# Performance work log

Measured on AMD Instinct MI355X. Metric: run time of the kernel, lower is better.

Reference implementation:

```python
import jax, jax.numpy as jnp
import numpy as np

D = 512          # hidden_dim
H_HEADS = 8
DH = D // H_HEADS  # 64
L = 6            # n_layers
P = 8            # patch size
KT = 3           # temporal kernel
Z_DIM = 32
FILM_SCALE = 0.5
ROPE_BASE = 10000.0
EPS = 1e-5


def layer_norm(x, g, b):
    mu = x.mean(-1, keepdims=True)
    var = ((x - mu) ** 2).mean(-1, keepdims=True)
    return (x - mu) * jax.lax.rsqrt(var + EPS) * g + b


def rotate_half(x):
    x1, x2 = jnp.split(x, 2, axis=-1)
    return jnp.concatenate([-x2, x1], axis=-1)


def rope_time(T, dtype):
    half = DH // 2
    inv_freq = ROPE_BASE ** (-(jnp.arange(half, dtype=dtype) / half))  # (half,)
    angles = jnp.arange(T, dtype=dtype)[:, None] * inv_freq[None, :]   # (T, half)
    sin = jnp.concatenate([jnp.sin(angles), jnp.sin(angles)], -1)      # (T, DH)
    cos = jnp.concatenate([jnp.cos(angles), jnp.cos(angles)], -1)
    return sin, cos


def setup_inputs() -> dict:
    key = jax.random.key(0)
    ks = iter(jax.random.split(key, 64))
    n = lambda shape, s=0.02: jax.random.normal(next(ks), shape, jnp.float32) * s
    inp = {
        "x": jax.random.normal(next(ks), (16, 32, 3, 64, 64), jnp.float32),
        "z": jax.random.normal(next(ks), (16, 32, Z_DIM), jnp.float32),
        # tokenizer: CausalConv3d (kt,ph,pw)=(3,8,8), stride (1,8,8)
        "conv_w": n((D, 3, KT, P, P)),
        "conv_b": jnp.zeros((D,), jnp.float32),
        "tok_g": jnp.ones((D,), jnp.float32),
        "tok_b": jnp.zeros((D,), jnp.float32),
        # FiLM from z -> (gamma, beta)
        "film_w": n((Z_DIM, 2 * D)),
        "film_b": jnp.zeros((2 * D,), jnp.float32),
        # transformer blocks (stacked over L)
        "ln1_g": jnp.ones((L, D), jnp.float32), "ln1_b": jnp.zeros((L, D), jnp.float32),
        "kqv_w": n((L, D, 3 * D)), "kqv_b": jnp.zeros((L, 3 * D), jnp.float32),
        "proj_w": n((L, D, D)), "proj_b": jnp.zeros((L, D), jnp.float32),
        "ln2_g": jnp.ones((L, D), jnp.float32), "ln2_b": jnp.zeros((L, D), jnp.float32),
        "mlp_w1": n((L, D, 4 * D)), "mlp_b1": jnp.zeros((L, 4 * D), jnp.float32),
        "mlp_w2": n((L, 4 * D, D)), "mlp_b2": jnp.zeros((L, D), jnp.float32),
        "rs_attn": jnp.full((L,), 0.5, jnp.float32),
        "rs_mlp": jnp.full((L,), 0.5, jnp.float32),
        # scoring head
        "head_g": jnp.ones((D,), jnp.float32), "head_b": jnp.zeros((D,), jnp.float32),
        "head_w": n((D, 1)), "head_bias": jnp.zeros((1,), jnp.float32),
    }
    return inp


def _forward(x, z, conv_w, conv_b, tok_g, tok_b, film_w, film_b,
             ln1_g, ln1_b, kqv_w, kqv_b, proj_w, proj_b, ln2_g, ln2_b,
             mlp_w1, mlp_b1, mlp_w2, mlp_b2, rs_attn, rs_mlp,
             head_g, head_b, head_w, head_bias):
    B, T, C, Himg, Wimg = x.shape
    # ---- SpatialTemporalTokenizer: causal Conv3d (pad time on past only) ----
    xc = jnp.transpose(x, (0, 2, 1, 3, 4))  # [B,C,T,H,W]
    y = jax.lax.conv_general_dilated(
        xc, conv_w, window_strides=(1, P, P),
        padding=[(KT - 1, 0), (0, 0), (0, 0)],
        dimension_numbers=("NCDHW", "OIDHW", "NCDHW"))
    y = y + conv_b[None, :, None, None, None]          # [B,D,T,Hn,Wn]
    Hn, Wn = y.shape[3], y.shape[4]
    tok = jnp.transpose(y, (0, 2, 3, 4, 1)).reshape(B, T, Hn * Wn, D)
    tok = layer_norm(tok, tok_g, tok_b)                 # [B,T,N,D]
    # ---- FiLM conditioning from z ----
    gb = z @ film_w + film_b                            # [B,T,2D]
    gamma, beta = jnp.split(gb, 2, axis=-1)
    tok = (1.0 + FILM_SCALE * gamma)[:, :, None, :] * tok + (FILM_SCALE * beta)[:, :, None, :]
    # ---- spatial pooling -> temporal sequence ----
    h = tok.mean(axis=2)                                # [B,T,D]
    # ---- transformer stack (causal, time RoPE, pre-LN, gated residuals) ----
    sin_t, cos_t = rope_time(T, h.dtype)                # (T, DH)
    causal = jnp.tril(jnp.ones((T, T), bool))
    neg_inf = jnp.finfo(h.dtype).min
    for i in range(L):
        xi = layer_norm(h, ln1_g[i], ln1_b[i])
        kqv = xi @ kqv_w[i] + kqv_b[i]                  # [B,T,3D]
        k, q, v = jnp.split(kqv, 3, axis=-1)            # torch chunk order: k,q,v
        sh = lambda t: t.reshape(B, T, H_HEADS, DH).transpose(0, 2, 1, 3)  # [B,h,T,d]
        q, k, v = sh(q), sh(k), sh(v)
        q = q * cos_t + rotate_half(q) * sin_t
        k = k * cos_t + rotate_half(k) * sin_t
        att = jnp.einsum("bhqd,bhkd->bhqk", q, k) / np.sqrt(DH)
        att = jnp.where(causal[None, None], att, neg_inf)
        att = jax.nn.softmax(att, axis=-1)
        yv = jnp.einsum("bhqk,bhkd->bhqd", att, v)
        yv = yv.transpose(0, 2, 1, 3).reshape(B, T, D)
        attn_out = yv @ proj_w[i] + proj_b[i]
        h = h + rs_attn[i] * attn_out
        x2 = layer_norm(h, ln2_g[i], ln2_b[i])
        m = jax.nn.gelu(x2 @ mlp_w1[i] + mlp_b1[i], approximate=False) @ mlp_w2[i] + mlp_b2[i]
        h = h + rs_mlp[i] * m
    # ---- per-timestep score head ----
    h = layer_norm(h, head_g, head_b)
    score = (h @ head_w + head_bias)[..., 0]            # [B,T]
    return score


def reference(x, z, conv_w, conv_b, tok_g, tok_b, film_w, film_b,
              ln1_g, ln1_b, kqv_w, kqv_b, proj_w, proj_b, ln2_g, ln2_b,
              mlp_w1, mlp_b1, mlp_w2, mlp_b2, rs_attn, rs_mlp,
              head_g, head_b, head_w, head_bias):
    return _forward(x, z, conv_w, conv_b, tok_g, tok_b, film_w, film_b,
                    ln1_g, ln1_b, kqv_w, kqv_b, proj_w, proj_b, ln2_g, ln2_b,
                    mlp_w1, mlp_b1, mlp_w2, mlp_b2, rs_attn, rs_mlp,
                    head_g, head_b, head_w, head_bias)
```

## Files before the change

kernel.cpp:

```cpp
#include <hip/hip_runtime.h>
#include <math.h>

#define EPS 1e-5f

typedef __attribute__((ext_vector_type(8))) short short8;
typedef __attribute__((ext_vector_type(4))) float f32x4;

__device__ __forceinline__ short f2bf(float f) {
    unsigned u = __float_as_uint(f);
    u += 0x7fffu + ((u >> 16) & 1u);
    return (short)(u >> 16);
}
__device__ __forceinline__ float bf2f(short s) {
    return __uint_as_float(((unsigned)(unsigned short)s) << 16);
}
__device__ __forceinline__ void async16(const void* g, void* l) {
    __builtin_amdgcn_global_load_lds(
        (const __attribute__((address_space(1))) unsigned*)g,
        (__attribute__((address_space(3))) unsigned*)l, 16, 0, 0);
}

__device__ __forceinline__ float block_reduce_sum_256(float v, float* red) {
    #pragma unroll
    for (int o = 32; o > 0; o >>= 1) v += __shfl_down(v, o, 64);
    __syncthreads();
    if ((threadIdx.x & 63) == 0) red[threadIdx.x >> 6] = v;
    __syncthreads();
    return red[0] + red[1] + red[2] + red[3];
}

__global__ __launch_bounds__(256) void prep_all(
    const float* __restrict__ z, const float* __restrict__ fw,
    const float* __restrict__ fb, float* __restrict__ gb,
    const float* __restrict__ conv_w, short* __restrict__ wbf,
    const float* __restrict__ x, short* __restrict__ xbf,
    float* __restrict__ ropeS, float* __restrict__ ropeC,
    const float* __restrict__ kqv_w, short* __restrict__ kqvT,
    const float* __restrict__ proj_w, short* __restrict__ projT,
    const float* __restrict__ mlp_w1, short* __restrict__ mlp1T,
    const float* __restrict__ mlp_w2, short* __restrict__ mlp2T) {
    int bi = blockIdx.x, tid = threadIdx.x;
    if (bi < 512) {
        __shared__ float zs[32];
        if (tid < 32) zs[tid] = z[bi * 32 + tid];
        __syncthreads();
        for (int j = tid; j < 1024; j += 256) {
            float acc = fb[j];
            #pragma unroll
            for (int k = 0; k < 32; k++) acc = fmaf(zs[k], fw[k * 1024 + j], acc);
            gb[bi * 1024 + j] = acc;
        }
        return;
    }
    if (bi < 1664) {
        int i = (bi - 512) * 256 + tid;
        wbf[i] = f2bf(conv_w[i]);
        return;
    }
    if (bi < 4736) {
        int i = (bi - 1664) * 256 + tid;
        float4 a = *(const float4*)(x + (size_t)i * 8);
        float4 b = *(const float4*)(x + (size_t)i * 8 + 4);
        short8 o = {f2bf(a.x), f2bf(a.y), f2bf(a.z), f2bf(a.w),
                    f2bf(b.x), f2bf(b.y), f2bf(b.z), f2bf(b.w)};
        *(short8*)(xbf + (size_t)i * 8) = o;
        return;
    }
    if (bi < 4740) {
        int idx = (bi - 4736) * 256 + tid;
        if (idx < 1024) {
            int t = idx >> 5, j = idx & 31;
            float ang = (float)t * expf(-(float)j * (logf(10000.f) / 32.f));
            ropeS[idx] = sinf(ang);
            ropeC[idx] = cosf(ang);
        }
        return;
    }
    __shared__ float tile[32][33];
    int rel0 = bi - 4740;
    const float* src; short* dst; int NT, K, N, rel;
    if (rel0 < 4608)       { src = kqv_w;  dst = kqvT;  NT = 48; K = 512;  N = 1536; rel = rel0; }
    else if (rel0 < 6144)  { src = proj_w; dst = projT; NT = 16; K = 512;  N = 512;  rel = rel0 - 4608; }
    else if (rel0 < 12288) { src = mlp_w1; dst = mlp1T; NT = 64; K = 512;  N = 2048; rel = rel0 - 6144; }
    else                   { src = mlp_w2; dst = mlp2T; NT = 16; K = 2048; N = 512;  rel = rel0 - 12288; }
    int per = NT * (K / 32);
    int layer = rel / per, r2 = rel - layer * per;
    int nt = r2 % NT, kt = r2 / NT;
    src += (size_t)layer * K * N;
    dst += (size_t)layer * N * K;
    int n0 = nt * 32, k0 = kt * 32;
    int lx = tid & 31, ly = tid >> 5;
    #pragma unroll
    for (int i = 0; i < 32; i += 8)
        tile[ly + i][lx] = src[(size_t)(k0 + ly + i) * N + n0 + lx];
    __syncthreads();
    if (tid < 128) {
        int row = tid >> 2, c = tid & 3;
        short8 o;
        #pragma unroll
        for (int j = 0; j < 8; j++) o[j] = f2bf(tile[c * 8 + j][row]);
        *(short8*)(dst + (size_t)(n0 + row) * K + k0 + c * 8) = o;
    }
}

__global__ __launch_bounds__(256, 2) void conv_fused(
    const short* __restrict__ xbf, const short* __restrict__ wbf,
    const float* __restrict__ cb, const float* __restrict__ tg,
    const float* __restrict__ tb, const float* __restrict__ gb,
    float* __restrict__ h) {
    __shared__ short As[64 * 32];
    __shared__ short Bs[512 * 32];
    __shared__ float redsum[4][64], redss[4][64];
    __shared__ float mu_s[64], inv_s[64];
    int bt = blockIdx.x, b = bt >> 5, t = bt & 31;
    int tid = threadIdx.x;
    int wave = tid >> 6, lane = tid & 63, quad = lane >> 4, l16 = lane & 15;

    int rowA = tid >> 2;
    int cA = (tid & 3) ^ ((rowA >> 1) & 3);
    int hn = rowA >> 3, wn2 = rowA & 7;
    long long baseA = (((long long)(b * 32 + t - 2) * 3) << 12)
                      + (long long)(hn * 8) * 64 + wn2 * 8;

    f32x4 acc[4][8];
    #pragma unroll
    for (int mt = 0; mt < 4; mt++)
        #pragma unroll
        for (int nt = 0; nt < 8; nt++) acc[mt][nt] = (f32x4){0.f, 0.f, 0.f, 0.f};

    for (int k0 = 0; k0 < 576; k0 += 32) {
        #pragma unroll
        for (int e = 0; e < 8; e++) {
            int s = e * 256 + tid;
            int n = s >> 2;
            int c = (s & 3) ^ ((n >> 1) & 3);
            async16(wbf + (size_t)n * 576 + k0 + c * 8, Bs + s * 8);
        }
        {
            int ks = (k0 >> 3) + cA;
            int ch = (ks >= 24) + (ks >= 48);
            int r = ks - ch * 24;
            int kt = r >> 3, ph = r & 7;
            short8 v8 = (short8){0, 0, 0, 0, 0, 0, 0, 0};
            if (t + kt >= 2)
                v8 = *(const short8*)(xbf + baseA
                        + ((long long)(kt * 3 + ch) << 12) + ph * 64);
            *(short8*)(As + tid * 8) = v8;
        }
        __syncthreads();
        short8 af[4], bf[8];
        #pragma unroll
        for (int mt = 0; mt < 4; mt++) {
            int row = mt * 16 + l16;
            int pc = quad ^ ((row >> 1) & 3);
            af[mt] = *(const short8*)(As + row * 32 + pc * 8);
        }
        #pragma unroll
        for (int nt = 0; nt < 8; nt++) {
            int row = wave * 128 + nt * 16 + l16;
            int pc = quad ^ ((row >> 1) & 3);
            bf[nt] = *(const short8*)(Bs + row * 32 + pc * 8);
        }
        #pragma unroll
        for (int mt = 0; mt < 4; mt++)
            #pragma unroll
            for (int nt = 0; nt < 8; nt++)
                acc[mt][nt] = __builtin_amdgcn_mfma_f32_16x16x32_bf16(
                    af[mt], bf[nt], acc[mt][nt], 0, 0, 0);
        __syncthreads();
    }

    float cbn[8], tgn[8], tbn[8], Gn[8], Ben[8];
    #pragma unroll
    for (int nt = 0; nt < 8; nt++) {
        int n = wave * 128 + nt * 16 + l16;
        cbn[nt] = cb[n]; tgn[nt] = tg[n]; tbn[nt] = tb[n];
        Gn[nt]  = 1.f + 0.5f * gb[bt * 1024 + n];
        Ben[nt] = 0.5f * gb[bt * 1024 + 512 + n];
    }
    #pragma unroll
    for (int mt = 0; mt < 4; mt++)
        #pragma unroll
        for (int reg = 0; reg < 4; reg++) {
            float s = 0.f, ss = 0.f;
            #pragma unroll
            for (int nt = 0; nt < 8; nt++) {
                float v = acc[mt][nt][reg] + cbn[nt];
                s += v; ss += v * v;
            }
            #pragma unroll
            for (int o = 1; o < 16; o <<= 1) {
                s  += __shfl_xor(s, o, 64);
                ss += __shfl_xor(ss, o, 64);
            }
            if (l16 == 0) {
                int m = mt * 16 + quad * 4 + reg;
                redsum[wave][m] = s; redss[wave][m] = ss;
            }
        }
    __syncthreads();
    if (tid < 64) {
        float S  = redsum[0][tid] + redsum[1][tid] + redsum[2][tid] + redsum[3][tid];
        float SS = redss[0][tid] + redss[1][tid] + redss[2][tid] + redss[3][tid];
        float mu = S * (1.f / 512.f);
        float var = SS * (1.f / 512.f) - mu * mu;
        mu_s[tid] = mu; inv_s[tid] = rsqrtf(var + EPS);
    }
    __syncthreads();
    float hacc[8] = {0.f, 0.f, 0.f, 0.f, 0.f, 0.f, 0.f, 0.f};
    #pragma unroll
    for (int mt = 0; mt < 4; mt++)
        #pragma unroll
        for (int reg = 0; reg < 4; reg++) {
            int m = mt * 16 + quad * 4 + reg;
            float mu = mu_s[m], inv = inv_s[m];
            #pragma unroll
            for (int nt = 0; nt < 8; nt++) {
                float v = acc[mt][nt][reg] + cbn[nt];
                hacc[nt] += (v - mu) * inv;
            }
        }
    #pragma unroll
    for (int nt = 0; nt < 8; nt++) {
        hacc[nt] += __shfl_xor(hacc[nt], 16, 64);
        hacc[nt] += __shfl_xor(hacc[nt], 32, 64);
    }
    if (quad == 0)
        #pragma unroll
        for (int nt = 0; nt < 8; nt++) {
            int n = wave * 128 + nt * 16 + l16;
            h[bt * 512 + n] = Gn[nt] * (tgn[nt] * (hacc[nt] * (1.f / 64.f)) + tbn[nt])
                              + Ben[nt];
        }
}

__global__ __launch_bounds__(256) void attn_fused(
    const float* __restrict__ hsrc, const float* __restrict__ lng,
    const float* __restrict__ lnb, const short* __restrict__ Bw,
    const float* __restrict__ bias, const float* __restrict__ ropeS,
    const float* __restrict__ ropeC, short* __restrict__ yv) {
    __shared__ char smem[57344] __attribute__((aligned(16)));
    __shared__ float mu_s[32], inv_s[32];
    short* As = (short*)smem;
    short* BsB[2] = {(short*)(smem + 32768), (short*)(smem + 45056)};
    float (*qsf)[64] = (float(*)[64])(smem);
    float (*ksf)[64] = (float(*)[64])(smem + 8192);
    short* vT  = (short*)(smem + 16384);
    short* qrb = (short*)(smem + 20480);
    short* krb = (short*)(smem + 24576);
    float (*att)[33] = (float(*)[33])(smem + 28672);
    short* pA  = (short*)(smem + 36864);
    int blk = blockIdx.x, b = blk >> 3, hh = blk & 7;
    int tid = threadIdx.x;
    int m0 = b * 32;
    {
        int row = tid >> 3, l8 = tid & 7;
        const float* hp = hsrc + (size_t)(m0 + row) * 512 + l8 * 64;
        float s = 0.f, ss = 0.f;
        #pragma unroll
        for (int i = 0; i < 16; i++) {
            float4 v = *(const float4*)(hp + i * 4);
            s += v.x + v.y + v.z + v.w;
            ss += v.x * v.x + v.y * v.y + v.z * v.z + v.w * v.w;
        }
        s += __shfl_xor(s, 1, 64); ss += __shfl_xor(ss, 1, 64);
        s += __shfl_xor(s, 2, 64); ss += __shfl_xor(ss, 2, 64);
        s += __shfl_xor(s, 4, 64); ss += __shfl_xor(ss, 4, 64);
        if (l8 == 0) {
            float mu = s * (1.f / 512.f);
            float var = ss * (1.f / 512.f) - mu * mu;
            mu_s[row] = mu;
            inv_s[row] = rsqrtf(var + EPS);
        }
    }
    #pragma unroll
    for (int e = 0; e < 3; e++) {
        int p = e * 256 + tid;
        int row = p >> 2, seg = (p & 3) ^ ((row >> 1) & 3);
        int n = ((row >> 6) << 9) + hh * 64 + (row & 63);
        async16(Bw + (size_t)n * 512 + seg * 8, BsB[0] + p * 8);
    }
    __syncthreads();
    #pragma unroll
    for (int e = 0; e < 8; e++) {
        int lc = e * 256 + tid;
        int row = lc >> 6, cc = lc & 63;
        float mu = mu_s[row], inv = inv_s[row];
        const float* hp = hsrc + (size_t)(m0 + row) * 512 + cc * 8;
        float4 a = *(const float4*)hp, b2 = *(const float4*)(hp + 4);
        float4 g0 = *(const float4*)(lng + cc * 8), g1 = *(const float4*)(lng + cc * 8 + 4);
        float4 b0 = *(const float4*)(lnb + cc * 8), b1 = *(const float4*)(lnb + cc * 8 + 4);
        short8 o = {f2bf((a.x - mu) * inv * g0.x + b0.x),
                    f2bf((a.y - mu) * inv * g0.y + b0.y),
                    f2bf((a.z - mu) * inv * g0.z + b0.z),
                    f2bf((a.w - mu) * inv * g0.w + b0.w),
                    f2bf((b2.x - mu) * inv * g1.x + b1.x),
                    f2bf((b2.y - mu) * inv * g1.y + b1.y),
                    f2bf((b2.z - mu) * inv * g1.z + b1.z),
                    f2bf((b2.w - mu) * inv * g1.w + b1.w)};
        *(short8*)(As + (row * 64 + (cc ^ (row & 7))) * 8) = o;
    }
    __syncthreads();
    int wave = tid >> 6, lane = tid & 63, quad = lane >> 4, l16 = lane & 15;
    f32x4 acc[2][3];
    #pragma unroll
    for (int m2 = 0; m2 < 2; m2++)
        #pragma unroll
        for (int g = 0; g < 3; g++) acc[m2][g] = (f32x4){0.f, 0.f, 0.f, 0.f};
    for (int it = 0; it < 16; it++) {
        short* Bsc = BsB[it & 1];
        if (it < 15) {
            int k0n = (it + 1) * 32;
            short* Bsn = BsB[(it + 1) & 1];
            #pragma unroll
            for (int e = 0; e < 3; e++) {
                int p = e * 256 + tid;
                int row = p >> 2, seg = (p & 3) ^ ((row >> 1) & 3);
                int n = ((row >> 6) << 9) + hh * 64 + (row & 63);
                async16(Bw + (size_t)n * 512 + k0n + seg * 8, Bsn + p * 8);
            }
        }
        int cc = it * 4 + quad;
        short8 af[2], bf[3];
        #pragma unroll
        for (int m2 = 0; m2 < 2; m2++) {
            int row = m2 * 16 + l16;
            af[m2] = *(const short8*)(As + (row * 64 + (cc ^ (row & 7))) * 8);
        }
        #pragma unroll
        for (int g = 0; g < 3; g++) {
            int row = g * 64 + wave * 16 + l16;
            int pc = quad ^ ((row >> 1) & 3);
            bf[g] = *(const short8*)(Bsc + (row * 4 + pc) * 8);
        }
        #pragma unroll
        for (int m2 = 0; m2 < 2; m2++)
            #pragma unroll
            for (int g = 0; g < 3; g++)
                acc[m2][g] = __builtin_amdgcn_mfma_f32_16x16x32_bf16(
                    af[m2], bf[g], acc[m2][g], 0, 0, 0);
        __syncthreads();
    }
    float bb0 = bias[hh * 64 + wave * 16 + l16];
    float bb1 = bias[512 + hh * 64 + wave * 16 + l16];
    float bb2 = bias[1024 + hh * 64 + wave * 16 + l16];
    int dcol = wave * 16 + l16;
    #pragma unroll
    for (int m2 = 0; m2 < 2; m2++)
        #pragma unroll
        for (int reg = 0; reg < 4; reg++) {
            int tkn = m2 * 16 + quad * 4 + reg;
            ksf[tkn][dcol] = acc[m2][0][reg] + bb0;
            qsf[tkn][dcol] = acc[m2][1][reg] + bb1;
            vT[dcol * 32 + (((tkn >> 3) ^ (dcol & 3)) << 3) + (tkn & 7)]
                = f2bf(acc[m2][2][reg] + bb2);
        }
    __syncthreads();
    #pragma unroll
    for (int e = 0; e < 8; e++) {
        int idx = e * 256 + tid;
        int t = idx >> 6, d = idx & 63, j = d & 31;
        float sv = ropeS[t * 32 + j], cv = ropeC[t * 32 + j];
        float qv = qsf[t][d], kv = ksf[t][d];
        float qo = qsf[t][d ^ 32], ko = ksf[t][d ^ 32];
        float rq = (d < 32) ? -qo : qo;
        float rk = (d < 32) ? -ko : ko;
        int addr = t * 64 + (((d >> 3) ^ (t & 7)) << 3) + (d & 7);
        qrb[addr] = f2bf(qv * cv + rq * sv);
        krb[addr] = f2bf(kv * cv + rk * sv);
    }
    __syncthreads();
    int mw = wave & 1, nw = wave >> 1;
    {
        f32x4 sc = (f32x4){0.f, 0.f, 0.f, 0.f};
        #pragma unroll
        for (int kc = 0; kc < 2; kc++) {
            int rq = mw * 16 + l16;
            int rk = nw * 16 + l16;
            short8 aq = *(const short8*)(qrb + rq * 64 + ((((kc << 2) + quad) ^ (rq & 7)) << 3));
            short8 bk = *(const short8*)(krb + rk * 64 + ((((kc << 2) + quad) ^ (rk & 7)) << 3));
            sc = __builtin_amdgcn_mfma_f32_16x16x32_bf16(aq, bk, sc, 0, 0, 0);
        }
        #pragma unroll
        for (int reg = 0; reg < 4; reg++) {
            int qt = mw * 16 + quad * 4 + reg;
            int kt = nw * 16 + l16;
            att[qt][kt] = (kt > qt) ? -1e30f : sc[reg] * 0.125f;
        }
    }
    __syncthreads();
    {
        int row = tid >> 3, g = tid & 7;
        float v0 = att[row][g * 4], v1 = att[row][g * 4 + 1];
        float v2 = att[row][g * 4 + 2], v3 = att[row][g * 4 + 3];
        float mx = fmaxf(fmaxf(v0, v1), fmaxf(v2, v3));
        mx = fmaxf(mx, __shfl_xor(mx, 1, 64));
        mx = fmaxf(mx, __shfl_xor(mx, 2, 64));
        mx = fmaxf(mx, __shfl_xor(mx, 4, 64));
        float e0 = expf(v0 - mx), e1 = expf(v1 - mx);
        float e2 = expf(v2 - mx), e3 = expf(v3 - mx);
        float s = e0 + e1 + e2 + e3;
        s += __shfl_xor(s, 1, 64);
        s += __shfl_xor(s, 2, 64);
        s += __shfl_xor(s, 4, 64);
        float inv = 1.f / s;
        short* pp = pA + row * 32 + g * 4;
        pp[0] = f2bf(e0 * inv); pp[1] = f2bf(e1 * inv);
        pp[2] = f2bf(e2 * inv); pp[3] = f2bf(e3 * inv);
    }
    __syncthreads();
    {
        int rp = mw * 16 + l16;
        short8 ap = *(const short8*)(pA + rp * 32 + quad * 8);
        #pragma unroll
        for (int i = 0; i < 2; i++) {
            int nt = (wave >> 1) * 2 + i;
            int rv = nt * 16 + l16;
            short8 bv = *(const short8*)(vT + rv * 32 + (((quad ^ (rv & 3))) << 3));
            f32x4 o = (f32x4){0.f, 0.f, 0.f, 0.f};
            o = __builtin_amdgcn_mfma_f32_16x16x32_bf16(ap, bv, o, 0, 0, 0);
            #pragma unroll
            for (int reg = 0; reg < 4; reg++) {
                int t = mw * 16 + quad * 4 + reg;
                int d = nt * 16 + l16;
                yv[(size_t)(b * 32 + t) * 512 + hh * 64 + d] = f2bf(o[reg]);
            }
        }
    }
}

__global__ __launch_bounds__(256) void gemm_ln(
    const float* __restrict__ hsrc, const float* __restrict__ lng,
    const float* __restrict__ lnb, const short* __restrict__ Bw,
    const float* __restrict__ bias, int N, int mode,
    float* __restrict__ outf, short* __restrict__ outb) {
    __shared__ short As[32 * 512];
    __shared__ short Bs[128 * 128];
    __shared__ float mu_s[32], inv_s[32];
    int tid = threadIdx.x;
    int m0 = blockIdx.y * 32, n0 = blockIdx.x * 128;
    {
        int row = tid >> 3, l8 = tid & 7;
        const float* hp = hsrc + (size_t)(m0 + row) * 512 + l8 * 64;
        float s = 0.f, ss = 0.f;
        #pragma unroll
        for (int i = 0; i < 16; i++) {
            float4 v = *(const float4*)(hp + i * 4);
            s += v.x + v.y + v.z + v.w;
            ss += v.x * v.x + v.y * v.y + v.z * v.z + v.w * v.w;
        }
        s += __shfl_xor(s, 1, 64); ss += __shfl_xor(ss, 1, 64);
        s += __shfl_xor(s, 2, 64); ss += __shfl_xor(ss, 2, 64);
        s += __shfl_xor(s, 4, 64); ss += __shfl_xor(ss, 4, 64);
        if (l8 == 0) {
            float mu = s * (1.f / 512.f);
            float var = ss * (1.f / 512.f) - mu * mu;
            mu_s[row] = mu;
            inv_s[row] = rsqrtf(var + EPS);
        }
    }
    #pragma unroll
    for (int e = 0; e < 8; e++) {
        int p = e * 256 + tid;
        int row = p >> 4, seg = (p & 15) ^ (row & 15);
        async16(Bw + (size_t)(n0 + row) * 512 + seg * 8, Bs + p * 8);
    }
    __syncthreads();
    #pragma unroll
    for (int e = 0; e < 8; e++) {
        int lc = e * 256 + tid;
        int row = lc >> 6, cc = lc & 63;
        float mu = mu_s[row], inv = inv_s[row];
        const float* hp = hsrc + (size_t)(m0 + row) * 512 + cc * 8;
        float4 a = *(const float4*)hp, b = *(const float4*)(hp + 4);
        float4 g0 = *(const float4*)(lng + cc * 8), g1 = *(const float4*)(lng + cc * 8 + 4);
        float4 b0 = *(const float4*)(lnb + cc * 8), b1 = *(const float4*)(lnb + cc * 8 + 4);
        short8 o = {f2bf((a.x - mu) * inv * g0.x + b0.x),
                    f2bf((a.y - mu) * inv * g0.y + b0.y),
                    f2bf((a.z - mu) * inv * g0.z + b0.z),
                    f2bf((a.w - mu) * inv * g0.w + b0.w),
                    f2bf((b.x - mu) * inv * g1.x + b1.x),
                    f2bf((b.y - mu) * inv * g1.y + b1.y),
                    f2bf((b.z - mu) * inv * g1.z + b1.z),
                    f2bf((b.w - mu) * inv * g1.w + b1.w)};
        *(short8*)(As + (row * 64 + (cc ^ (row & 7))) * 8) = o;
    }
    __syncthreads();
    int wave = tid >> 6, lane = tid & 63, quad = lane >> 4, l16 = lane & 15;
    f32x4 acc[2][2];
    #pragma unroll
    for (int a2 = 0; a2 < 2; a2++)
        #pragma unroll
        for (int b2 = 0; b2 < 2; b2++) acc[a2][b2] = (f32x4){0.f, 0.f, 0.f, 0.f};
    for (int it = 0; it < 4; it++) {
        int k0 = it * 128;
        #pragma unroll
        for (int ksub = 0; ksub < 4; ksub++) {
            int ccb = ksub * 4 + quad;
            short8 af[2], bf[2];
            #pragma unroll
            for (int m2 = 0; m2 < 2; m2++) {
                int row = m2 * 16 + l16;
                int cc = (k0 >> 3) + ccb;
                af[m2] = *(const short8*)(As + (row * 64 + (cc ^ (row & 7))) * 8);
            }
            #pragma unroll
            for (int n2 = 0; n2 < 2; n2++) {
                int row = wave * 32 + n2 * 16 + l16;
                bf[n2] = *(const short8*)(Bs + (row * 16 + (ccb ^ (row & 15))) * 8);
            }
            #pragma unroll
            for (int m2 = 0; m2 < 2; m2++)
                #pragma unroll
                for (int n2 = 0; n2 < 2; n2++)
                    acc[m2][n2] = __builtin_amdgcn_mfma_f32_16x16x32_bf16(
                        af[m2], bf[n2], acc[m2][n2], 0, 0, 0);
        }
        __syncthreads();
        if (it < 3) {
            int k0n = (it + 1) * 128;
            #pragma unroll
            for (int e = 0; e < 8; e++) {
                int p = e * 256 + tid;
                int row = p >> 4, seg = (p & 15) ^ (row & 15);
                async16(Bw + (size_t)(n0 + row) * 512 + k0n + seg * 8, Bs + p * 8);
            }
            __syncthreads();
        }
    }
    #pragma unroll
    for (int m2 = 0; m2 < 2; m2++)
        #pragma unroll
        for (int n2 = 0; n2 < 2; n2++)
            #pragma unroll
            for (int reg = 0; reg < 4; reg++) {
                int m = m0 + m2 * 16 + quad * 4 + reg;
                int n = n0 + wave * 32 + n2 * 16 + l16;
                float v = acc[m2][n2][reg] + bias[n];
                if (mode == 1) {
                    v = 0.5f * v * (1.f + erff(v * 0.70710678118f));
                    outb[(size_t)m * N + n] = f2bf(v);
                } else {
                    outf[(size_t)m * N + n] = v;
                }
            }
}

__global__ __launch_bounds__(256) void gemm_res(
    const short* __restrict__ Ag, const short* __restrict__ Bw,
    const float* __restrict__ bias, const float* __restrict__ rsPtr,
    float* __restrict__ hm, int K, int Ks) {
    __shared__ short As[2][32 * 128];
    __shared__ short Bs[2][64 * 128];
    int tid = threadIdx.x;
    int m0 = blockIdx.y * 32, n0 = blockIdx.x * 64;
    int kbase = blockIdx.z * Ks;
    int wave = tid >> 6, lane = tid & 63, quad = lane >> 4, l16 = lane & 15;
    int nIter = Ks >> 7;
    f32x4 acc[2];
    acc[0] = (f32x4){0.f, 0.f, 0.f, 0.f};
    acc[1] = (f32x4){0.f, 0.f, 0.f, 0.f};
    auto stage = [&](int k0, int buf) {
        #pragma unroll
        for (int e = 0; e < 2; e++) {
            int p = e * 256 + tid;
            int row = p >> 4, seg = (p & 15) ^ (row & 15);
            async16(Ag + (size_t)(m0 + row) * K + k0 + seg * 8, As[buf] + p * 8);
        }
        #pragma unroll
        for (int e = 0; e < 4; e++) {
            int p = e * 256 + tid;
            int row = p >> 4, seg = (p & 15) ^ (row & 15);
            async16(Bw + (size_t)(n0 + row) * K + k0 + seg * 8, Bs[buf] + p * 8);
        }
    };
    stage(kbase, 0);
    __syncthreads();
    for (int it = 0; it < nIter; it++) {
        int cur = it & 1;
        if (it + 1 < nIter) stage(kbase + (it + 1) * 128, cur ^ 1);
        #pragma unroll
        for (int ksub = 0; ksub < 4; ksub++) {
            int ccb = ksub * 4 + quad;
            short8 bf;
            {
                int row = wave * 16 + l16;
                bf = *(const short8*)(Bs[cur] + (row * 16 + (ccb ^ (row & 15))) * 8);
            }
            #pragma unroll
            for (int m2 = 0; m2 < 2; m2++) {
                int row = m2 * 16 + l16;
                short8 af = *(const short8*)(As[cur] + (row * 16 + (ccb ^ (row & 15))) * 8);
                acc[m2] = __builtin_amdgcn_mfma_f32_16x16x32_bf16(af, bf, acc[m2], 0, 0, 0);
            }
        }
        __syncthreads();
    }
    float rsv = *rsPtr;
    bool addb = (blockIdx.z == 0);
    #pragma unroll
    for (int m2 = 0; m2 < 2; m2++)
        #pragma unroll
        for (int reg = 0; reg < 4; reg++) {
            int m = m0 + m2 * 16 + quad * 4 + reg;
            int n = n0 + wave * 16 + l16;
            float v = acc[m2][reg] + (addb ? bias[n] : 0.f);
            atomicAdd(&hm[(size_t)m * 512 + n], rsv * v);
        }
}

__global__ __launch_bounds__(256) void head_kernel(
    const float* __restrict__ h, const float* __restrict__ g,
    const float* __restrict__ bb, const float* __restrict__ w,
    const float* __restrict__ bias0, float* __restrict__ out) {
    __shared__ float red[8];
    int token = blockIdx.x, tid = threadIdx.x;
    float v0 = h[token * 512 + tid], v1 = h[token * 512 + tid + 256];
    float s  = block_reduce_sum_256(v0 + v1, red);
    float ss = block_reduce_sum_256(v0 * v0 + v1 * v1, red);
    float mu = s * (1.f / 512.f);
    float var = ss * (1.f / 512.f) - mu * mu;
    float inv = rsqrtf(var + EPS);
    float n0 = (v0 - mu) * inv * g[tid] + bb[tid];
    float n1 = (v1 - mu) * inv * g[tid + 256] + bb[tid + 256];
    float dot = block_reduce_sum_256(n0 * w[tid] + n1 * w[tid + 256], red);
    if (tid == 0) out[token] = dot + bias0[0];
}

extern "C" void kernel_launch(void* const* d_in, const int* in_sizes, int n_in,
                              void* d_out, int out_size, void* d_ws, size_t ws_size,
                              hipStream_t stream) {
    const float* x       = (const float*)d_in[0];
    const float* z       = (const float*)d_in[1];
    const float* conv_w  = (const float*)d_in[2];
    const float* conv_b  = (const float*)d_in[3];
    const float* tok_g   = (const float*)d_in[4];
    const float* tok_b   = (const float*)d_in[5];
    const float* film_w  = (const float*)d_in[6];
    const float* film_b  = (const float*)d_in[7];
    const float* ln1_g   = (const float*)d_in[8];
    const float* ln1_b   = (const float*)d_in[9];
    const float* kqv_w   = (const float*)d_in[10];
    const float* kqv_b   = (const float*)d_in[11];
    const float* proj_w  = (const float*)d_in[12];
    const float* proj_b  = (const float*)d_in[13];
    const float* ln2_g   = (const float*)d_in[14];
    const float* ln2_b   = (const float*)d_in[15];
    const float* mlp_w1  = (const float*)d_in[16];
    const float* mlp_b1  = (const float*)d_in[17];
    const float* mlp_w2  = (const float*)d_in[18];
    const float* mlp_b2  = (const float*)d_in[19];
    const float* rs_attn = (const float*)d_in[20];
    const float* rs_mlp  = (const float*)d_in[21];
    const float* head_g  = (const float*)d_in[22];
    const float* head_b  = (const float*)d_in[23];
    const float* head_w  = (const float*)d_in[24];
    const float* head_bs = (const float*)d_in[25];
    float* out = (float*)d_out;

    float* ws = (float*)d_ws;
    float* gb    = ws;
    float* h     = gb + 524288;
    float* ropeS = h + 262144;
    float* ropeC = ropeS + 1024;
    short* sb = (short*)(ropeC + 1024);
    short* wbf   = sb;
    short* kqvT  = wbf   + 294912;
    short* projT = kqvT  + 4718592;
    short* mlp1T = projT + 1572864;
    short* mlp2T = mlp1T + 6291456;
    short* yvb   = mlp2T + 6291456;
    short* mbuf  = yvb   + 262144;
    short* xbf   = mbuf  + 1048576;

    prep_all<<<23172, 256, 0, stream>>>(
        z, film_w, film_b, gb, conv_w, wbf, x, xbf, ropeS, ropeC,
        kqv_w, kqvT, proj_w, projT, mlp_w1, mlp1T, mlp_w2, mlp2T);

    conv_fused<<<512, 256, 0, stream>>>(xbf, wbf, conv_b, tok_g, tok_b, gb, h);

    for (int i = 0; i < 6; i++) {
        attn_fused<<<128, 256, 0, stream>>>(
            h, ln1_g + i * 512, ln1_b + i * 512,
            kqvT + (size_t)i * 1536 * 512, kqv_b + i * 1536, ropeS, ropeC, yvb);
        gemm_res<<<dim3(8, 16, 2), 256, 0, stream>>>(
            yvb, projT + (size_t)i * 512 * 512, proj_b + i * 512,
            rs_attn + i, h, 512, 256);
        gemm_ln<<<dim3(16, 16), 256, 0, stream>>>(
            h, ln2_g + i * 512, ln2_b + i * 512,
            mlp1T + (size_t)i * 2048 * 512, mlp_b1 + i * 2048,
            2048, 1, nullptr, mbuf);
        gemm_res<<<dim3(8, 16, 4), 256, 0, stream>>>(
            mbuf, mlp2T + (size_t)i * 512 * 2048, mlp_b2 + i * 512,
            rs_mlp + i, h, 2048, 512);
    }

    head_kernel<<<512, 256, 0, stream>>>(h, head_g, head_b, head_w, head_bs, out);
}
```

Before: 466.1 us.

## Fuse output projection into attention and MLP up/down into one kernel

```diff
diff --git a/kernel.cpp b/kernel.cpp
--- a/kernel.cpp
+++ b/kernel.cpp
@@ -234,11 +234,13 @@
         }
 }
 
-__global__ __launch_bounds__(256) void attn_fused(
-    const float* __restrict__ hsrc, const float* __restrict__ lng,
+__global__ __launch_bounds__(256) void attn_proj(
+    const float* __restrict__ rIn, const float* __restrict__ lng,
     const float* __restrict__ lnb, const short* __restrict__ Bw,
     const float* __restrict__ bias, const float* __restrict__ ropeS,
-    const float* __restrict__ ropeC, short* __restrict__ yv) {
+    const float* __restrict__ ropeC, const short* __restrict__ Pw,
+    const float* __restrict__ pbias, const float* __restrict__ rsPtr,
+    float* __restrict__ rMid) {
     __shared__ char smem[57344] __attribute__((aligned(16)));
     __shared__ float mu_s[32], inv_s[32];
     short* As = (short*)smem;
@@ -250,12 +252,14 @@
     short* krb = (short*)(smem + 24576);
     float (*att)[33] = (float(*)[33])(smem + 28672);
     short* pA  = (short*)(smem + 36864);
+    short* yA  = qrb;
+    short* PBs = (short*)(smem + 24576);
     int blk = blockIdx.x, b = blk >> 3, hh = blk & 7;
     int tid = threadIdx.x;
     int m0 = b * 32;
     {
         int row = tid >> 3, l8 = tid & 7;
-        const float* hp = hsrc + (size_t)(m0 + row) * 512 + l8 * 64;
+        const float* hp = rIn + (size_t)(m0 + row) * 512 + l8 * 64;
         float s = 0.f, ss = 0.f;
         #pragma unroll
         for (int i = 0; i < 16; i++) {
@@ -286,7 +290,7 @@
         int lc = e * 256 + tid;
         int row = lc >> 6, cc = lc & 63;
         float mu = mu_s[row], inv = inv_s[row];
-        const float* hp = hsrc + (size_t)(m0 + row) * 512 + cc * 8;
+        const float* hp = rIn + (size_t)(m0 + row) * 512 + cc * 8;
         float4 a = *(const float4*)hp, b2 = *(const float4*)(hp + 4);
         float4 g0 = *(const float4*)(lng + cc * 8), g1 = *(const float4*)(lng + cc * 8 + 4);
         float4 b0 = *(const float4*)(lnb + cc * 8), b1 = *(const float4*)(lnb + cc * 8 + 4);
@@ -423,25 +427,81 @@
             for (int reg = 0; reg < 4; reg++) {
                 int t = mw * 16 + quad * 4 + reg;
                 int d = nt * 16 + l16;
-                yv[(size_t)(b * 32 + t) * 512 + hh * 64 + d] = f2bf(o[reg]);
-            }
-        }
-    }
-}
-
-__global__ __launch_bounds__(256) void gemm_ln(
-    const float* __restrict__ hsrc, const float* __restrict__ lng,
-    const float* __restrict__ lnb, const short* __restrict__ Bw,
-    const float* __restrict__ bias, int N, int mode,
-    float* __restrict__ outf, short* __restrict__ outb) {
+                yA[(t * 8 + ((d >> 3) ^ (t & 7))) * 8 + (d & 7)] = f2bf(o[reg]);
+            }
+        }
+    }
+    __syncthreads();
+    float rsv = *rsPtr;
+    #pragma unroll
+    for (int hN = 0; hN < 2; hN++) {
+        #pragma unroll
+        for (int e = 0; e < 8; e++) {
+            int p = e * 256 + tid;
+            int row = p >> 3, seg = (p & 7) ^ (row & 7);
+            int n = hN * 256 + row;
+            async16(Pw + (size_t)n * 512 + hh * 64 + seg * 8, PBs + p * 8);
+        }
+        __syncthreads();
+        f32x4 accp[2][4];
+        #pragma unroll
+        for (int m2 = 0; m2 < 2; m2++)
+            #pragma unroll
+            for (int nt = 0; nt < 4; nt++) accp[m2][nt] = (f32x4){0.f, 0.f, 0.f, 0.f};
+        #pragma unroll
+        for (int ksub = 0; ksub < 2; ksub++) {
+            int ccb = ksub * 4 + quad;
+            short8 af[2];
+            #pragma unroll
+            for (int m2 = 0; m2 < 2; m2++) {
+                int row = m2 * 16 + l16;
+                af[m2] = *(const short8*)(yA + (row * 8 + (ccb ^ (row & 7))) * 8);
+            }
+            #pragma unroll
+            for (int nt = 0; nt < 4; nt++) {
+                int row = (wave * 4 + nt) * 16 + l16;
+                short8 bfr = *(const short8*)(PBs + (row * 8 + (ccb ^ (row & 7))) * 8);
+                #pragma unroll
+                for (int m2 = 0; m2 < 2; m2++)
+                    accp[m2][nt] = __builtin_amdgcn_mfma_f32_16x16x32_bf16(
+                        af[m2], bfr, accp[m2][nt], 0, 0, 0);
+            }
+        }
+        #pragma unroll
+        for (int m2 = 0; m2 < 2; m2++)
+            #pragma unroll
+            for (int nt = 0; nt < 4; nt++)
+                #pragma unroll
+                for (int reg = 0; reg < 4; reg++) {
+                    int m = m0 + m2 * 16 + quad * 4 + reg;
+                    int n = hN * 256 + (wave * 4 + nt) * 16 + l16;
+                    float add = rsv * accp[m2][nt][reg];
+                    if (hh == 0)
+                        add += rIn[(size_t)m * 512 + n] + rsv * pbias[n];
+                    atomicAdd(&rMid[(size_t)m * 512 + n], add);
+                }
+        __syncthreads();
+    }
+}
+
+__global__ __launch_bounds__(256) void mlp_fused(
+    const float* __restrict__ rMid, const float* __restrict__ lng,
+    const float* __restrict__ lnb, const short* __restrict__ W1,
+    const float* __restrict__ b1, const short* __restrict__ W2,
+    const float* __restrict__ b2, const float* __restrict__ rsPtr,
+    float* __restrict__ rOut) {
     __shared__ short As[32 * 512];
-    __shared__ short Bs[128 * 128];
+    __shared__ short Bs[256 * 64];
     __shared__ float mu_s[32], inv_s[32];
+    short* Bs2 = As;
+    short* A2 = Bs;
     int tid = threadIdx.x;
-    int m0 = blockIdx.y * 32, n0 = blockIdx.x * 128;
+    int ks = blockIdx.x, mt = blockIdx.y;
+    int m0 = mt * 32, c0 = ks * 256;
+    int wave = tid >> 6, lane = tid & 63, quad = lane >> 4, l16 = lane & 15;
     {
         int row = tid >> 3, l8 = tid & 7;
-        const float* hp = hsrc + (size_t)(m0 + row) * 512 + l8 * 64;
+        const float* hp = rMid + (size_t)(m0 + row) * 512 + l8 * 64;
         float s = 0.f, ss = 0.f;
         #pragma unroll
         for (int i = 0; i < 16; i++) {
@@ -459,45 +519,45 @@
             inv_s[row] = rsqrtf(var + EPS);
         }
     }
-    #pragma unroll
-    for (int e = 0; e < 8; e++) {
-        int p = e * 256 + tid;
-        int row = p >> 4, seg = (p & 15) ^ (row & 15);
-        async16(Bw + (size_t)(n0 + row) * 512 + seg * 8, Bs + p * 8);
-    }
     __syncthreads();
     #pragma unroll
     for (int e = 0; e < 8; e++) {
         int lc = e * 256 + tid;
         int row = lc >> 6, cc = lc & 63;
         float mu = mu_s[row], inv = inv_s[row];
-        const float* hp = hsrc + (size_t)(m0 + row) * 512 + cc * 8;
+        const float* hp = rMid + (size_t)(m0 + row) * 512 + cc * 8;
         float4 a = *(const float4*)hp, b = *(const float4*)(hp + 4);
         float4 g0 = *(const float4*)(lng + cc * 8), g1 = *(const float4*)(lng + cc * 8 + 4);
-        float4 b0 = *(const float4*)(lnb + cc * 8), b1 = *(const float4*)(lnb + cc * 8 + 4);
+        float4 b0 = *(const float4*)(lnb + cc * 8), b1v = *(const float4*)(lnb + cc * 8 + 4);
         short8 o = {f2bf((a.x - mu) * inv * g0.x + b0.x),
                     f2bf((a.y - mu) * inv * g0.y + b0.y),
                     f2bf((a.z - mu) * inv * g0.z + b0.z),
                     f2bf((a.w - mu) * inv * g0.w + b0.w),
-                    f2bf((b.x - mu) * inv * g1.x + b1.x),
-                    f2bf((b.y - mu) * inv * g1.y + b1.y),
-                    f2bf((b.z - mu) * inv * g1.z + b1.z),
-                    f2bf((b.w - mu) * inv * g1.w + b1.w)};
+                    f2bf((b.x - mu) * inv * g1.x + b1v.x),
+                    f2bf((b.y - mu) * inv * g1.y + b1v.y),
+                    f2bf((b.z - mu) * inv * g1.z + b1v.z),
+                    f2bf((b.w - mu) * inv * g1.w + b1v.w)};
         *(short8*)(As + (row * 64 + (cc ^ (row & 7))) * 8) = o;
     }
     __syncthreads();
-    int wave = tid >> 6, lane = tid & 63, quad = lane >> 4, l16 = lane & 15;
-    f32x4 acc[2][2];
-    #pragma unroll
-    for (int a2 = 0; a2 < 2; a2++)
-        #pragma unroll
-        for (int b2 = 0; b2 < 2; b2++) acc[a2][b2] = (f32x4){0.f, 0.f, 0.f, 0.f};
-    for (int it = 0; it < 4; it++) {
-        int k0 = it * 128;
-        #pragma unroll
-        for (int ksub = 0; ksub < 4; ksub++) {
+    f32x4 acc1[2][4];
+    #pragma unroll
+    for (int m2 = 0; m2 < 2; m2++)
+        #pragma unroll
+        for (int nt = 0; nt < 4; nt++) acc1[m2][nt] = (f32x4){0.f, 0.f, 0.f, 0.f};
+    for (int it = 0; it < 8; it++) {
+        int k0 = it * 64;
+        #pragma unroll
+        for (int e = 0; e < 8; e++) {
+            int p = e * 256 + tid;
+            int row = p >> 3, seg = (p & 7) ^ (row & 7);
+            async16(W1 + (size_t)(c0 + row) * 512 + k0 + seg * 8, Bs + p * 8);
+        }
+        __syncthreads();
+        #pragma unroll
+        for (int ksub = 0; ksub < 2; ksub++) {
             int ccb = ksub * 4 + quad;
-            short8 af[2], bf[2];
+            short8 af[2];
             #pragma unroll
             for (int m2 = 0; m2 < 2; m2++) {
                 int row = m2 * 16 + l16;
@@ -505,108 +565,84 @@
                 af[m2] = *(const short8*)(As + (row * 64 + (cc ^ (row & 7))) * 8);
             }
             #pragma unroll
-            for (int n2 = 0; n2 < 2; n2++) {
-                int row = wave * 32 + n2 * 16 + l16;
-                bf[n2] = *(const short8*)(Bs + (row * 16 + (ccb ^ (row & 15))) * 8);
-            }
-            #pragma unroll
-            for (int m2 = 0; m2 < 2; m2++)
+            for (int nt = 0; nt < 4; nt++) {
+                int row = (wave * 4 + nt) * 16 + l16;
+                short8 bfr = *(const short8*)(Bs + (row * 8 + (ccb ^ (row & 7))) * 8);
                 #pragma unroll
-                for (int n2 = 0; n2 < 2; n2++)
-                    acc[m2][n2] = __builtin_amdgcn_mfma_f32_16x16x32_bf16(
-                        af[m2], bf[n2], acc[m2][n2], 0, 0, 0);
+                for (int m2 = 0; m2 < 2; m2++)
+                    acc1[m2][nt] = __builtin_amdgcn_mfma_f32_16x16x32_bf16(
+                        af[m2], bfr, acc1[m2][nt], 0, 0, 0);
+            }
         }
         __syncthreads();
-        if (it < 3) {
-            int k0n = (it + 1) * 128;
+    }
+    #pragma unroll
+    for (int m2 = 0; m2 < 2; m2++)
+        #pragma unroll
+        for (int nt = 0; nt < 4; nt++)
+            #pragma unroll
+            for (int reg = 0; reg < 4; reg++) {
+                int row = m2 * 16 + quad * 4 + reg;
+                int n = (wave * 4 + nt) * 16 + l16;
+                float v = acc1[m2][nt][reg] + b1[c0 + n];
+                v = 0.5f * v * (1.f + erff(v * 0.70710678118f));
+                A2[(row * 32 + ((n >> 3) ^ (row & 7))) * 8 + (n & 7)] = f2bf(v);
+            }
+    __syncthreads();
+    float rsv = *rsPtr;
+    for (int g = 0; g < 4; g++) {
+        f32x4 acc2[2][2];
+        #pragma unroll
+        for (int m2 = 0; m2 < 2; m2++)
+            #pragma unroll
+            for (int nt = 0; nt < 2; nt++) acc2[m2][nt] = (f32x4){0.f, 0.f, 0.f, 0.f};
+        #pragma unroll
+        for (int kit = 0; kit < 2; kit++) {
+            int kk0 = kit * 128;
             #pragma unroll
             for (int e = 0; e < 8; e++) {
                 int p = e * 256 + tid;
                 int row = p >> 4, seg = (p & 15) ^ (row & 15);
-                async16(Bw + (size_t)(n0 + row) * 512 + k0n + seg * 8, Bs + p * 8);
+                async16(W2 + (size_t)(g * 128 + row) * 2048 + c0 + kk0 + seg * 8,
+                        Bs2 + p * 8);
             }
             __syncthreads();
-        }
-    }
-    #pragma unroll
-    for (int m2 = 0; m2 < 2; m2++)
-        #pragma unroll
-        for (int n2 = 0; n2 < 2; n2++)
-            #pragma unroll
-            for (int reg = 0; reg < 4; reg++) {
-                int m = m0 + m2 * 16 + quad * 4 + reg;
-                int n = n0 + wave * 32 + n2 * 16 + l16;
-                float v = acc[m2][n2][reg] + bias[n];
-                if (mode == 1) {
-                    v = 0.5f * v * (1.f + erff(v * 0.70710678118f));
-                    outb[(size_t)m * N + n] = f2bf(v);
-                } else {
-                    outf[(size_t)m * N + n] = v;
+            #pragma unroll
+            for (int ksub = 0; ksub < 4; ksub++) {
+                int ccb = ksub * 4 + quad;
+                short8 af[2];
+                #pragma unroll
+                for (int m2 = 0; m2 < 2; m2++) {
+                    int row = m2 * 16 + l16;
+                    int cc = (kk0 >> 3) + ccb;
+                    af[m2] = *(const short8*)(A2 + (row * 32 + (cc ^ (row & 7))) * 8);
                 }
-            }
-}
-
-__global__ __launch_bounds__(256) void gemm_res(
-    const short* __restrict__ Ag, const short* __restrict__ Bw,
-    const float* __restrict__ bias, const float* __restrict__ rsPtr,
-    float* __restrict__ hm, int K, int Ks) {
-    __shared__ short As[2][32 * 128];
-    __shared__ short Bs[2][64 * 128];
-    int tid = threadIdx.x;
-    int m0 = blockIdx.y * 32, n0 = blockIdx.x * 64;
-    int kbase = blockIdx.z * Ks;
-    int wave = tid >> 6, lane = tid & 63, quad = lane >> 4, l16 = lane & 15;
-    int nIter = Ks >> 7;
-    f32x4 acc[2];
-    acc[0] = (f32x4){0.f, 0.f, 0.f, 0.f};
-    acc[1] = (f32x4){0.f, 0.f, 0.f, 0.f};
-    auto stage = [&](int k0, int buf) {
-        #pragma unroll
-        for (int e = 0; e < 2; e++) {
-            int p = e * 256 + tid;
-            int row = p >> 4, seg = (p & 15) ^ (row & 15);
-            async16(Ag + (size_t)(m0 + row) * K + k0 + seg * 8, As[buf] + p * 8);
-        }
-        #pragma unroll
-        for (int e = 0; e < 4; e++) {
-            int p = e * 256 + tid;
-            int row = p >> 4, seg = (p & 15) ^ (row & 15);
-            async16(Bw + (size_t)(n0 + row) * K + k0 + seg * 8, Bs[buf] + p * 8);
-        }
-    };
-    stage(kbase, 0);
-    __syncthreads();
-    for (int it = 0; it < nIter; it++) {
-        int cur = it & 1;
-        if (it + 1 < nIter) stage(kbase + (it + 1) * 128, cur ^ 1);
-        #pragma unroll
-        for (int ksub = 0; ksub < 4; ksub++) {
-            int ccb = ksub * 4 + quad;
-            short8 bf;
-            {
-                int row = wave * 16 + l16;
-                bf = *(const short8*)(Bs[cur] + (row * 16 + (ccb ^ (row & 15))) * 8);
-            }
-            #pragma unroll
-            for (int m2 = 0; m2 < 2; m2++) {
-                int row = m2 * 16 + l16;
-                short8 af = *(const short8*)(As[cur] + (row * 16 + (ccb ^ (row & 15))) * 8);
-                acc[m2] = __builtin_amdgcn_mfma_f32_16x16x32_bf16(af, bf, acc[m2], 0, 0, 0);
-            }
-        }
-        __syncthreads();
-    }
-    float rsv = *rsPtr;
-    bool addb = (blockIdx.z == 0);
-    #pragma unroll
-    for (int m2 = 0; m2 < 2; m2++)
-        #pragma unroll
-        for (int reg = 0; reg < 4; reg++) {
-            int m = m0 + m2 * 16 + quad * 4 + reg;
-            int n = n0 + wave * 16 + l16;
-            float v = acc[m2][reg] + (addb ? bias[n] : 0.f);
-            atomicAdd(&hm[(size_t)m * 512 + n], rsv * v);
-        }
+                #pragma unroll
+                for (int nt = 0; nt < 2; nt++) {
+                    int row = (wave * 2 + nt) * 16 + l16;
+                    short8 bfr = *(const short8*)(Bs2 + (row * 16 + (ccb ^ (row & 15))) * 8);
+                    #pragma unroll
+                    for (int m2 = 0; m2 < 2; m2++)
+                        acc2[m2][nt] = __builtin_amdgcn_mfma_f32_16x16x32_bf16(
+                            af[m2], bfr, acc2[m2][nt], 0, 0, 0);
+                }
+            }
+            __syncthreads();
+        }
+        #pragma unroll
+        for (int m2 = 0; m2 < 2; m2++)
+            #pragma unroll
+            for (int nt = 0; nt < 2; nt++)
+                #pragma unroll
+                for (int reg = 0; reg < 4; reg++) {
+                    int m = m0 + m2 * 16 + quad * 4 + reg;
+                    int n = g * 128 + (wave * 2 + nt) * 16 + l16;
+                    float add = rsv * acc2[m2][nt][reg];
+                    if (ks == 0)
+                        add += rMid[(size_t)m * 512 + n] + rsv * b2[n];
+                    atomicAdd(&rOut[(size_t)m * 512 + n], add);
+                }
+    }
 }
 
 __global__ __launch_bounds__(256) void head_kernel(
@@ -660,8 +696,9 @@
 
     float* ws = (float*)d_ws;
     float* gb    = ws;
-    float* h     = gb + 524288;
-    float* ropeS = h + 262144;
+    float* r0    = gb + 524288;
+    float* rbufs = r0 + 262144;
+    float* ropeS = rbufs + 12 * 262144;
     float* ropeC = ropeS + 1024;
     short* sb = (short*)(ropeC + 1024);
     short* wbf   = sb;
@@ -669,31 +706,30 @@
     short* projT = kqvT  + 4718592;
     short* mlp1T = projT + 1572864;
     short* mlp2T = mlp1T + 6291456;
-    short* yvb   = mlp2T + 6291456;
-    short* mbuf  = yvb   + 262144;
-    short* xbf   = mbuf  + 1048576;
+    short* xbf   = mlp2T + 6291456;
 
     prep_all<<<23172, 256, 0, stream>>>(
         z, film_w, film_b, gb, conv_w, wbf, x, xbf, ropeS, ropeC,
         kqv_w, kqvT, proj_w, projT, mlp_w1, mlp1T, mlp_w2, mlp2T);
-
-    conv_fused<<<512, 256, 0, stream>>>(xbf, wbf, conv_b, tok_g, tok_b, gb, h);
-
+    hipMemsetAsync(rbufs, 0, (size_t)12 * 262144 * 4, stream);
+
+    conv_fused<<<512, 256, 0, stream>>>(xbf, wbf, conv_b, tok_g, tok_b, gb, r0);
+
+    const float* rIn = r0;
     for (int i = 0; i < 6; i++) {
-        attn_fused<<<128, 256, 0, stream>>>(
-            h, ln1_g + i * 512, ln1_b + i * 512,
-            kqvT + (size_t)i * 1536 * 512, kqv_b + i * 1536, ropeS, ropeC, yvb);
-        gemm_res<<<dim3(8, 16, 2), 256, 0, stream>>>(
-            yvb, projT + (size_t)i * 512 * 512, proj_b + i * 512,
-            rs_attn + i, h, 512, 256);
-        gemm_ln<<<dim3(16, 16), 256, 0, stream>>>(
-            h, ln2_g + i * 512, ln2_b + i * 512,
+        float* rMid = rbufs + (size_t)(2 * i) * 262144;
+        float* rOut = rbufs + (size_t)(2 * i + 1) * 262144;
+        attn_proj<<<128, 256, 0, stream>>>(
+            rIn, ln1_g + i * 512, ln1_b + i * 512,
+            kqvT + (size_t)i * 1536 * 512, kqv_b + i * 1536, ropeS, ropeC,
+            projT + (size_t)i * 512 * 512, proj_b + i * 512, rs_attn + i, rMid);
+        mlp_fused<<<dim3(8, 16), 256, 0, stream>>>(
+            rMid, ln2_g + i * 512, ln2_b + i * 512,
             mlp1T + (size_t)i * 2048 * 512, mlp_b1 + i * 2048,
-            2048, 1, nullptr, mbuf);
-        gemm_res<<<dim3(8, 16, 4), 256, 0, stream>>>(
-            mbuf, mlp2T + (size_t)i * 512 * 2048, mlp_b2 + i * 512,
-            rs_mlp + i, h, 2048, 512);
-    }
-
-    head_kernel<<<512, 256, 0, stream>>>(h, head_g, head_b, head_w, head_bs, out);
-}
+            mlp2T + (size_t)i * 512 * 2048, mlp_b2 + i * 512,
+            rs_mlp + i, rOut);
+        rIn = rOut;
+    }
+
+    head_kernel<<<512, 256, 0, stream>>>(rIn, head_g, head_b, head_w, head_bs, out);
+}
```

Result: slower. 727.1 us (+56.0%).
